# Kernel tuning notes

Measured on AMD Instinct MI355X. Metric: run time of the kernel, lower is better.

Reference implementation:

```python
import jax, jax.numpy as jnp
import numpy as np

EPS = 1e-6
H = 12  # heads

def layernorm(x, alpha, bias):
    # Faithful to source: unbiased std (ddof=1) and division by (std + eps)
    mean = jnp.mean(x, axis=-1, keepdims=True)
    std = jnp.std(x, axis=-1, ddof=1, keepdims=True)
    return alpha * (x - mean) / (std + EPS) + bias

def setup_inputs() -> dict:
    key = jax.random.key(0)
    ks = jax.random.split(key, 8)
    B, S, D, F = 2, 2048, 768, 3072
    w_scale = 0.02  # keep activations in a sane range
    return {
        "x": jax.random.normal(ks[0], (B, S, D), dtype=jnp.float32),
        "src_mask": jnp.ones((B, 1, 1, S), dtype=jnp.int32),
        "wq": jax.random.normal(ks[1], (D, D), dtype=jnp.float32) * w_scale,
        "wk": jax.random.normal(ks[2], (D, D), dtype=jnp.float32) * w_scale,
        "wv": jax.random.normal(ks[3], (D, D), dtype=jnp.float32) * w_scale,
        "wo": jax.random.normal(ks[4], (D, D), dtype=jnp.float32) * w_scale,
        "w1": jax.random.normal(ks[5], (D, F), dtype=jnp.float32) * w_scale,
        "b1": jnp.zeros((F,), dtype=jnp.float32),
        "w2": jax.random.normal(ks[6], (F, D), dtype=jnp.float32) * w_scale,
        "b2": jnp.zeros((D,), dtype=jnp.float32),
        "ln1_alpha": jnp.ones((1,), dtype=jnp.float32),
        "ln1_bias": jnp.zeros((1,), dtype=jnp.float32),
        "ln2_alpha": jnp.ones((1,), dtype=jnp.float32),
        "ln2_bias": jnp.zeros((1,), dtype=jnp.float32),
    }

def reference(x, src_mask, wq, wk, wv, wo, w1, b1, w2, b2,
              ln1_alpha, ln1_bias, ln2_alpha, ln2_bias):
    B, S, D = x.shape
    dk = D // H
    # ---- residual 1: pre-LN self-attention ----
    t = layernorm(x, ln1_alpha, ln1_bias)
    q = (t @ wq).reshape(B, S, H, dk).transpose(0, 2, 1, 3)  # [B,H,S,dk]
    k = (t @ wk).reshape(B, S, H, dk).transpose(0, 2, 1, 3)
    v = (t @ wv).reshape(B, S, H, dk).transpose(0, 2, 1, 3)
    scores = jnp.einsum('bhqd,bhkd->bhqk', q, k) / jnp.sqrt(jnp.float32(dk))
    # Faithful to source quirk: masked positions are SET to 1e-9 (not -inf)
    scores = jnp.where(src_mask == 0, jnp.float32(1e-9), scores)
    attn = jax.nn.softmax(scores, axis=-1)
    o = jnp.einsum('bhqk,bhkd->bhqd', attn, v)
    o = o.transpose(0, 2, 1, 3).reshape(B, S, D) @ wo
    x = x + o
    # ---- residual 2: pre-LN FFN ----
    t = layernorm(x, ln2_alpha, ln2_bias)
    ffn = jax.nn.relu(t @ w1 + b1) @ w2 + b2
    return x + ffn
```

## Files before the change

### kernel.cpp

```cpp
#include <hip/hip_runtime.h>

#define AS1 __attribute__((address_space(1)))
#define AS3 __attribute__((address_space(3)))

typedef float f32x4 __attribute__((ext_vector_type(4)));
typedef __bf16 bf16x8 __attribute__((ext_vector_type(8)));

__device__ __forceinline__ unsigned short f2bf(float f) {
    union { float f; unsigned u; } v; v.f = f;
    unsigned r = v.u + 0x7fffu + ((v.u >> 16) & 1u);
    return (unsigned short)(r >> 16);
}

__device__ __forceinline__ void async16(const void* g, void* l) {
    __builtin_amdgcn_global_load_lds((AS1 void*)g, (AS3 void*)l, 16, 0, 0);
}

#define SWZ4(r) ((((r) & 3) ^ (((r) >> 2) & 3)))

__global__ void transpose_cvt(const float* __restrict__ W, unsigned short* __restrict__ Wt,
                              int K, int N) {
    __shared__ float tile[32][33];
    int n0 = blockIdx.x * 32, k0 = blockIdx.y * 32;
    int tx = threadIdx.x, ty = threadIdx.y;
#pragma unroll
    for (int i = 0; i < 32; i += 8)
        tile[ty + i][tx] = W[(size_t)(k0 + ty + i) * N + n0 + tx];
    __syncthreads();
#pragma unroll
    for (int i = 0; i < 32; i += 8)
        Wt[(size_t)(n0 + ty + i) * K + k0 + tx] = f2bf(tile[tx][ty + i]);
}

__global__ __launch_bounds__(256) void ln_kernel(const float* __restrict__ x,
                                                 unsigned short* __restrict__ t,
                                                 const float* __restrict__ alpha,
                                                 const float* __restrict__ bias) {
    const int row = blockIdx.x;
    const float* xr = x + (size_t)row * 768;
    float v[3], sum = 0.f, ss = 0.f;
#pragma unroll
    for (int i = 0; i < 3; i++) {
        v[i] = xr[threadIdx.x + 256 * i];
        sum += v[i]; ss += v[i] * v[i];
    }
#pragma unroll
    for (int off = 32; off; off >>= 1) {
        sum += __shfl_down(sum, off);
        ss  += __shfl_down(ss, off);
    }
    __shared__ float s1[4], s2[4];
    int wid = threadIdx.x >> 6, lane = threadIdx.x & 63;
    if (lane == 0) { s1[wid] = sum; s2[wid] = ss; }
    __syncthreads();
    if (threadIdx.x == 0) {
        float a = 0.f, b = 0.f;
#pragma unroll
        for (int i = 0; i < 4; i++) { a += s1[i]; b += s2[i]; }
        s1[0] = a; s2[0] = b;
    }
    __syncthreads();
    sum = s1[0]; ss = s2[0];
    float mean = sum * (1.f / 768.f);
    float var = (ss - sum * mean) * (1.f / 767.f);
    float sc = alpha[0] / (sqrtf(fmaxf(var, 0.f)) + 1e-6f);
    float bs = bias[0];
#pragma unroll
    for (int i = 0; i < 3; i++)
        t[(size_t)row * 768 + threadIdx.x + 256 * i] = f2bf(sc * (v[i] - mean) + bs);
}

template <int MODE>
__global__ __launch_bounds__(256, 2) void gemm_bt(
    const unsigned short* __restrict__ A, const unsigned short* __restrict__ Bt,
    int M, int N, int K, const float* __restrict__ bias,
    const float* __restrict__ res, void* __restrict__ outp) {
    __shared__ __align__(16) unsigned short As[128 * 32];
    __shared__ __align__(16) unsigned short Bs[128 * 32];
    const int tid = threadIdx.x;
    const int lane = tid & 63, w = tid >> 6;
    const int wm = w & 1, wn = w >> 1;
    const int m0 = blockIdx.y * 128, n0 = blockIdx.x * 128;
    const int quad = lane >> 4, l16 = lane & 15;

    const int s0 = (2 * w) * 64 + lane;
    const int r0 = s0 >> 2, g0 = s0 & 3;
    const int s1 = s0 + 64;
    const int r1 = s1 >> 2, g1 = s1 & 3;
    const unsigned short* gA0 = A  + (size_t)(m0 + r0) * K + ((g0 ^ SWZ4(r0)) * 8);
    const unsigned short* gA1 = A  + (size_t)(m0 + r1) * K + ((g1 ^ SWZ4(r1)) * 8);
    const unsigned short* gB0 = Bt + (size_t)(n0 + r0) * K + ((g0 ^ SWZ4(r0)) * 8);
    const unsigned short* gB1 = Bt + (size_t)(n0 + r1) * K + ((g1 ^ SWZ4(r1)) * 8);
    unsigned short* lA0 = As + (2 * w) * 512;
    unsigned short* lA1 = As + (2 * w + 1) * 512;
    unsigned short* lB0 = Bs + (2 * w) * 512;
    unsigned short* lB1 = Bs + (2 * w + 1) * 512;

    f32x4 acc[4][4];
    const f32x4 z = {0.f, 0.f, 0.f, 0.f};
#pragma unroll
    for (int mt = 0; mt < 4; mt++)
#pragma unroll
        for (int nt = 0; nt < 4; nt++) acc[mt][nt] = z;

    const int nK = K >> 5;
    for (int kt = 0; kt < nK; ++kt) {
        __syncthreads();
        async16(gA0, lA0); async16(gA1, lA1);
        async16(gB0, lB0); async16(gB1, lB1);
        gA0 += 32; gA1 += 32; gB0 += 32; gB1 += 32;
        __syncthreads();
        bf16x8 af[4], bf[4];
#pragma unroll
        for (int mt = 0; mt < 4; mt++) {
            int r = 64 * wm + 16 * mt + l16;
            af[mt] = *(const bf16x8*)&As[r * 32 + ((quad ^ SWZ4(r)) * 8)];
        }
#pragma unroll
        for (int nt = 0; nt < 4; nt++) {
            int r = 64 * wn + 16 * nt + l16;
            bf[nt] = *(const bf16x8*)&Bs[r * 32 + ((quad ^ SWZ4(r)) * 8)];
        }
#pragma unroll
        for (int mt = 0; mt < 4; mt++)
#pragma unroll
            for (int nt = 0; nt < 4; nt++)
                acc[mt][nt] = __builtin_amdgcn_mfma_f32_16x16x32_bf16(af[mt], bf[nt], acc[mt][nt], 0, 0, 0);
    }

#pragma unroll
    for (int mt = 0; mt < 4; mt++) {
#pragma unroll
        for (int nt = 0; nt < 4; nt++) {
            const int col = n0 + 64 * wn + 16 * nt + l16;
            float bv = 0.f;
            if (MODE == 1 || MODE == 3) bv = bias[col];
#pragma unroll
            for (int r = 0; r < 4; r++) {
                const int row = m0 + 64 * wm + 16 * mt + quad * 4 + r;
                const size_t idx = (size_t)row * N + col;
                const float v = acc[mt][nt][r];
                if (MODE == 0) ((unsigned short*)outp)[idx] = f2bf(v);
                else if (MODE == 1) ((unsigned short*)outp)[idx] = f2bf(fmaxf(v + bv, 0.f));
                else if (MODE == 2) ((float*)outp)[idx] = v + res[idx];
                else ((float*)outp)[idx] = v + bv + res[idx];
            }
        }
    }
}

template <int MODE>
__global__ __launch_bounds__(256, 3) void gemm64_bt(
    const unsigned short* __restrict__ A, const unsigned short* __restrict__ Bt,
    int M, int N, int K, const float* __restrict__ bias,
    const float* __restrict__ res, void* __restrict__ outp) {
    __shared__ __align__(16) unsigned short As[64 * 32];
    __shared__ __align__(16) unsigned short Bs[64 * 32];
    const int tid = threadIdx.x;
    const int lane = tid & 63, w = tid >> 6;
    const int m0 = blockIdx.y * 64, n0 = blockIdx.x * 64;
    const int quad = lane >> 4, l16 = lane & 15;

    const int sl = w * 64 + lane;
    const int r = sl >> 2, g = sl & 3;
    const unsigned short* gA = A  + (size_t)(m0 + r) * K + ((g ^ SWZ4(r)) * 8);
    const unsigned short* gB = Bt + (size_t)(n0 + r) * K + ((g ^ SWZ4(r)) * 8);
    unsigned short* lA = As + w * 512;
    unsigned short* lB = Bs + w * 512;

    f32x4 acc[4];
    const f32x4 z = {0.f, 0.f, 0.f, 0.f};
#pragma unroll
    for (int nt = 0; nt < 4; nt++) acc[nt] = z;

    const int nK = K >> 5;
    for (int kt = 0; kt < nK; ++kt) {
        __syncthreads();
        async16(gA, lA); async16(gB, lB);
        gA += 32; gB += 32;
        __syncthreads();
        const int ra = 16 * w + l16;
        bf16x8 af = *(const bf16x8*)&As[ra * 32 + ((quad ^ SWZ4(ra)) * 8)];
#pragma unroll
        for (int nt = 0; nt < 4; nt++) {
            int rb = 16 * nt + l16;
            bf16x8 bf = *(const bf16x8*)&Bs[rb * 32 + ((quad ^ SWZ4(rb)) * 8)];
            acc[nt] = __builtin_amdgcn_mfma_f32_16x16x32_bf16(af, bf, acc[nt], 0, 0, 0);
        }
    }

#pragma unroll
    for (int nt = 0; nt < 4; nt++) {
        const int col = n0 + 16 * nt + l16;
        float bv = 0.f;
        if (MODE == 1 || MODE == 3) bv = bias[col];
#pragma unroll
        for (int rr = 0; rr < 4; rr++) {
            const int row = m0 + 16 * w + quad * 4 + rr;
            const size_t idx = (size_t)row * N + col;
            const float v = acc[nt][rr];
            if (MODE == 0) ((unsigned short*)outp)[idx] = f2bf(v);
            else if (MODE == 1) ((unsigned short*)outp)[idx] = f2bf(fmaxf(v + bv, 0.f));
            else if (MODE == 2) ((float*)outp)[idx] = v + res[idx];
            else ((float*)outp)[idx] = v + bv + res[idx];
        }
    }
}

__global__ void v_transpose(const unsigned short* __restrict__ qkvc,
                            unsigned short* __restrict__ vt) {
    __shared__ unsigned short t[64][65];
    const int bh = blockIdx.y, b = bh / 12, h = bh % 12;
    const int s0 = blockIdx.x * 64;
    const int tx = threadIdx.x, ty = threadIdx.y;
#pragma unroll
    for (int i = 0; i < 64; i += 4)
        t[ty + i][tx] = qkvc[(size_t)(b * 2048 + s0 + ty + i) * 2304 + 1536 + h * 64 + tx];
    __syncthreads();
#pragma unroll
    for (int i = 0; i < 64; i += 4)
        vt[((size_t)bh * 64 + ty + i) * 2048 + s0 + tx] = t[tx][ty + i];
}

__global__ __launch_bounds__(256, 3) void flash_attn(
    const unsigned short* __restrict__ qkvc,
    const unsigned short* __restrict__ vt,
    const int* __restrict__ mask,
    unsigned short* __restrict__ attno) {
    const int bh = blockIdx.y, b = bh / 12, h = bh % 12;
    const int s0 = blockIdx.x * 64;
    __shared__ __align__(16) unsigned short UQP[4 * 16 * 136];
    __shared__ __align__(16) unsigned short Ks[128 * 64];
    __shared__ __align__(16) unsigned short Vs[64 * 128];
    __shared__ int Ms[128];
    const int tid = threadIdx.x, lane = tid & 63, w = tid >> 6;
    const int quad = lane >> 4, l16 = lane & 15;

    {
        int sl0 = (2 * w) * 64 + lane;
        int r0 = sl0 >> 3, g0 = sl0 & 7;
        int sl1 = sl0 + 64;
        int r1 = sl1 >> 3, g1 = sl1 & 7;
        async16(qkvc + (size_t)(b * 2048 + s0 + r0) * 2304 + h * 64 + ((g0 ^ (r0 & 7)) * 8),
                UQP + (2 * w) * 512);
        async16(qkvc + (size_t)(b * 2048 + s0 + r1) * 2304 + h * 64 + ((g1 ^ (r1 & 7)) * 8),
                UQP + (2 * w + 1) * 512);
    }
    __syncthreads();
    bf16x8 aQ[2];
    {
        int r = 16 * w + l16;
#pragma unroll
        for (int kk = 0; kk < 2; kk++)
            aQ[kk] = *(const bf16x8*)&UQP[r * 64 + (((kk * 4 + quad) ^ (r & 7)) * 8)];
    }
    __bf16* Ps = (__bf16*)(UQP + w * (16 * 136));

    f32x4 Oacc[4], Lacc;
    const f32x4 z = {0.f, 0.f, 0.f, 0.f};
#pragma unroll
    for (int nt = 0; nt < 4; nt++) Oacc[nt] = z;
    Lacc = z;
    bf16x8 ones;
#pragma unroll
    for (int i = 0; i < 8; i++) ones[i] = (__bf16)1.0f;

    const unsigned short* kbase = qkvc + 768;
    const unsigned short* vbase = vt + (size_t)bh * 64 * 2048;
    const float SCL = 0.125f * 1.44269504088896340736f;
    const float MSK = 1.4426950408889634e-9f;

    for (int j = 0; j < 16; j++) {
        const int k0 = j * 128;
        __syncthreads();
#pragma unroll
        for (int c = 0; c < 4; c++) {
            int sl = (4 * w + c) * 64 + lane;
            int r = sl >> 3, g = sl & 7;
            async16(kbase + (size_t)(b * 2048 + k0 + r) * 2304 + h * 64 + ((g ^ (r & 7)) * 8),
                    Ks + (4 * w + c) * 512);
        }
#pragma unroll
        for (int c = 0; c < 4; c++) {
            int sl = (4 * w + c) * 64 + lane;
            int r = sl >> 4, g = sl & 15;
            async16(vbase + (size_t)r * 2048 + k0 + ((g ^ (r & 15)) * 8),
                    Vs + (4 * w + c) * 512);
        }
        if (tid < 128) Ms[tid] = mask[b * 2048 + k0 + tid];
        __syncthreads();

        f32x4 sc[8];
#pragma unroll
        for (int nt = 0; nt < 8; nt++) {
            int rr = nt * 16 + l16;
            bf16x8 bk0 = *(const bf16x8*)&Ks[rr * 64 + (((0 + quad) ^ (rr & 7)) * 8)];
            bf16x8 bk1 = *(const bf16x8*)&Ks[rr * 64 + (((4 + quad) ^ (rr & 7)) * 8)];
            sc[nt] = __builtin_amdgcn_mfma_f32_16x16x32_bf16(aQ[0], bk0, z, 0, 0, 0);
            sc[nt] = __builtin_amdgcn_mfma_f32_16x16x32_bf16(aQ[1], bk1, sc[nt], 0, 0, 0);
        }
#pragma unroll
        for (int nt = 0; nt < 8; nt++) {
            const int msk = Ms[nt * 16 + l16];
#pragma unroll
            for (int r = 0; r < 4; r++) {
                float v = msk ? sc[nt][r] * SCL : MSK;
                sc[nt][r] = __builtin_amdgcn_exp2f(v);
            }
        }
#pragma unroll
        for (int nt = 0; nt < 8; nt++)
#pragma unroll
            for (int r = 0; r < 4; r++)
                Ps[(quad * 4 + r) * 136 + nt * 16 + l16] = (__bf16)sc[nt][r];

#pragma unroll
        for (int ktile = 0; ktile < 4; ktile++) {
            bf16x8 aP = *(const bf16x8*)&Ps[l16 * 136 + ktile * 32 + quad * 8];
            Lacc = __builtin_amdgcn_mfma_f32_16x16x32_bf16(aP, ones, Lacc, 0, 0, 0);
#pragma unroll
            for (int nt = 0; nt < 4; nt++) {
                int rr = nt * 16 + l16;
                bf16x8 bv = *(const bf16x8*)&Vs[rr * 128 + (((ktile * 4 + quad) ^ (rr & 15)) * 8)];
                Oacc[nt] = __builtin_amdgcn_mfma_f32_16x16x32_bf16(aP, bv, Oacc[nt], 0, 0, 0);
            }
        }
    }

    float inv[4];
#pragma unroll
    for (int r = 0; r < 4; r++) inv[r] = 1.0f / Lacc[r];
#pragma unroll
    for (int nt = 0; nt < 4; nt++)
#pragma unroll
        for (int r = 0; r < 4; r++) {
            const int row = s0 + 16 * w + quad * 4 + r;
            attno[(size_t)(b * 2048 + row) * 768 + h * 64 + nt * 16 + l16] =
                f2bf(Oacc[nt][r] * inv[r]);
        }
}

extern "C" void kernel_launch(void* const* d_in, const int* in_sizes, int n_in,
                              void* d_out, int out_size, void* d_ws, size_t ws_size,
                              hipStream_t stream) {
    const float* x    = (const float*)d_in[0];
    const int*   mask = (const int*)d_in[1];
    const float* wq   = (const float*)d_in[2];
    const float* wk   = (const float*)d_in[3];
    const float* wv   = (const float*)d_in[4];
    const float* wo   = (const float*)d_in[5];
    const float* w1   = (const float*)d_in[6];
    const float* b1   = (const float*)d_in[7];
    const float* w2   = (const float*)d_in[8];
    const float* b2   = (const float*)d_in[9];
    const float* ln1a = (const float*)d_in[10];
    const float* ln1b = (const float*)d_in[11];
    const float* ln2a = (const float*)d_in[12];
    const float* ln2b = (const float*)d_in[13];

    char* p = (char*)d_ws;
    auto carve = [&](size_t bytes) {
        char* q = p;
        p += (bytes + 255) & ~(size_t)255;
        return q;
    };
    unsigned short* wTqkv = (unsigned short*)carve((size_t)2304 * 768 * 2);
    unsigned short* wTo   = (unsigned short*)carve((size_t)768 * 768 * 2);
    unsigned short* wT1   = (unsigned short*)carve((size_t)3072 * 768 * 2);
    unsigned short* wT2   = (unsigned short*)carve((size_t)768 * 3072 * 2);
    unsigned short* vtb   = (unsigned short*)carve((size_t)24 * 64 * 2048 * 2);
    float*          x1    = (float*)carve((size_t)4096 * 768 * 4);
    char* unionA = carve((size_t)4096 * 768 * 2 + (size_t)4096 * 2304 * 2);
    unsigned short* t1   = (unsigned short*)unionA;
    unsigned short* qkvc = (unsigned short*)(unionA + (size_t)4096 * 768 * 2);
    unsigned short* ffnh = (unsigned short*)unionA;
    unsigned short* attno = (unsigned short*)carve((size_t)4096 * 768 * 2);
    unsigned short* t2 = attno;

    dim3 tb(32, 8);
    transpose_cvt<<<dim3(24, 24), tb, 0, stream>>>(wq, wTqkv, 768, 768);
    transpose_cvt<<<dim3(24, 24), tb, 0, stream>>>(wk, wTqkv + (size_t)768 * 768, 768, 768);
    transpose_cvt<<<dim3(24, 24), tb, 0, stream>>>(wv, wTqkv + (size_t)1536 * 768, 768, 768);
    transpose_cvt<<<dim3(24, 24), tb, 0, stream>>>(wo, wTo, 768, 768);
    transpose_cvt<<<dim3(96, 24), tb, 0, stream>>>(w1, wT1, 768, 3072);
    transpose_cvt<<<dim3(24, 96), tb, 0, stream>>>(w2, wT2, 3072, 768);

    ln_kernel<<<4096, 256, 0, stream>>>(x, t1, ln1a, ln1b);
    gemm_bt<0><<<dim3(18, 32), 256, 0, stream>>>(t1, wTqkv, 4096, 2304, 768,
                                                 nullptr, nullptr, qkvc);
    v_transpose<<<dim3(32, 24), dim3(64, 4), 0, stream>>>(qkvc, vtb);
    flash_attn<<<dim3(32, 24), 256, 0, stream>>>(qkvc, vtb, mask, attno);
    gemm64_bt<2><<<dim3(12, 64), 256, 0, stream>>>(attno, wTo, 4096, 768, 768,
                                                   nullptr, x, x1);
    ln_kernel<<<4096, 256, 0, stream>>>(x1, t2, ln2a, ln2b);
    gemm_bt<1><<<dim3(24, 32), 256, 0, stream>>>(t2, wT1, 4096, 3072, 768,
                                                 b1, nullptr, ffnh);
    gemm64_bt<3><<<dim3(12, 64), 256, 0, stream>>>(ffnh, wT2, 4096, 768, 3072,
                                                   b2, x1, (float*)d_out);
}
```

Before: 306.9 us.

## Double-buffer GEMM LDS tiles with register prefetch, one barrier per k-step

Both GEMM kernels switch from direct global-to-LDS async loads with two barriers per k-step to register-staged prefetch into double-buffered LDS with a single waitcnt+barrier. The next tile's global loads are issued before the current tile's MFMAs, aiming to hide global latency and halve barrier count. The 64x64 kernel also widens its K step from 32 to 64 using an 8-way XOR swizzle, and the 128 kernel's occupancy hint rises from 2 to 3 blocks. The trade-off is more registers for staging, double the LDS footprint, and a possible spill or occupancy loss under the tighter launch bound.

```diff
diff --git a/kernel.cpp b/kernel.cpp
--- a/kernel.cpp
+++ b/kernel.cpp
@@ -1,7 +1,4 @@
 #include <hip/hip_runtime.h>
-
-#define AS1 __attribute__((address_space(1)))
-#define AS3 __attribute__((address_space(3)))
 
 typedef float f32x4 __attribute__((ext_vector_type(4)));
 typedef __bf16 bf16x8 __attribute__((ext_vector_type(8)));
@@ -12,8 +9,14 @@
     return (unsigned short)(r >> 16);
 }
 
+#define AS1 __attribute__((address_space(1)))
+#define AS3 __attribute__((address_space(3)))
 __device__ __forceinline__ void async16(const void* g, void* l) {
     __builtin_amdgcn_global_load_lds((AS1 void*)g, (AS3 void*)l, 16, 0, 0);
+}
+
+__device__ __forceinline__ void sync_lds() {
+    asm volatile("s_waitcnt lgkmcnt(0)\n\ts_barrier" ::: "memory");
 }
 
 #define SWZ4(r) ((((r) & 3) ^ (((r) >> 2) & 3)))
@@ -71,30 +74,26 @@
 }
 
 template <int MODE>
-__global__ __launch_bounds__(256, 2) void gemm_bt(
+__global__ __launch_bounds__(256, 3) void gemm_bt(
     const unsigned short* __restrict__ A, const unsigned short* __restrict__ Bt,
     int M, int N, int K, const float* __restrict__ bias,
     const float* __restrict__ res, void* __restrict__ outp) {
-    __shared__ __align__(16) unsigned short As[128 * 32];
-    __shared__ __align__(16) unsigned short Bs[128 * 32];
+    __shared__ __align__(16) unsigned short As[2][128 * 32];
+    __shared__ __align__(16) unsigned short Bs[2][128 * 32];
     const int tid = threadIdx.x;
     const int lane = tid & 63, w = tid >> 6;
     const int wm = w & 1, wn = w >> 1;
     const int m0 = blockIdx.y * 128, n0 = blockIdx.x * 128;
     const int quad = lane >> 4, l16 = lane & 15;
 
-    const int s0 = (2 * w) * 64 + lane;
-    const int r0 = s0 >> 2, g0 = s0 & 3;
-    const int s1 = s0 + 64;
-    const int r1 = s1 >> 2, g1 = s1 & 3;
-    const unsigned short* gA0 = A  + (size_t)(m0 + r0) * K + ((g0 ^ SWZ4(r0)) * 8);
-    const unsigned short* gA1 = A  + (size_t)(m0 + r1) * K + ((g1 ^ SWZ4(r1)) * 8);
-    const unsigned short* gB0 = Bt + (size_t)(n0 + r0) * K + ((g0 ^ SWZ4(r0)) * 8);
-    const unsigned short* gB1 = Bt + (size_t)(n0 + r1) * K + ((g1 ^ SWZ4(r1)) * 8);
-    unsigned short* lA0 = As + (2 * w) * 512;
-    unsigned short* lA1 = As + (2 * w + 1) * 512;
-    unsigned short* lB0 = Bs + (2 * w) * 512;
-    unsigned short* lB1 = Bs + (2 * w + 1) * 512;
+    const int r0 = tid >> 2, g0 = tid & 3;
+    const int r1 = r0 + 64, g1 = g0;
+    const unsigned short* gA0 = A  + (size_t)(m0 + r0) * K + g0 * 8;
+    const unsigned short* gA1 = A  + (size_t)(m0 + r1) * K + g1 * 8;
+    const unsigned short* gB0 = Bt + (size_t)(n0 + r0) * K + g0 * 8;
+    const unsigned short* gB1 = Bt + (size_t)(n0 + r1) * K + g1 * 8;
+    const int wA0 = r0 * 32 + ((g0 ^ SWZ4(r0)) * 8);
+    const int wA1 = r1 * 32 + ((g1 ^ SWZ4(r1)) * 8);
 
     f32x4 acc[4][4];
     const f32x4 z = {0.f, 0.f, 0.f, 0.f};
@@ -103,23 +102,32 @@
 #pragma unroll
         for (int nt = 0; nt < 4; nt++) acc[mt][nt] = z;
 
+    bf16x8 ra0 = *(const bf16x8*)gA0, ra1 = *(const bf16x8*)gA1;
+    bf16x8 rb0 = *(const bf16x8*)gB0, rb1 = *(const bf16x8*)gB1;
+    gA0 += 32; gA1 += 32; gB0 += 32; gB1 += 32;
+
     const int nK = K >> 5;
     for (int kt = 0; kt < nK; ++kt) {
-        __syncthreads();
-        async16(gA0, lA0); async16(gA1, lA1);
-        async16(gB0, lB0); async16(gB1, lB1);
-        gA0 += 32; gA1 += 32; gB0 += 32; gB1 += 32;
-        __syncthreads();
+        unsigned short* Ac = As[kt & 1];
+        unsigned short* Bc = Bs[kt & 1];
+        *(bf16x8*)&Ac[wA0] = ra0; *(bf16x8*)&Ac[wA1] = ra1;
+        *(bf16x8*)&Bc[wA0] = rb0; *(bf16x8*)&Bc[wA1] = rb1;
+        if (kt + 1 < nK) {
+            ra0 = *(const bf16x8*)gA0; ra1 = *(const bf16x8*)gA1;
+            rb0 = *(const bf16x8*)gB0; rb1 = *(const bf16x8*)gB1;
+            gA0 += 32; gA1 += 32; gB0 += 32; gB1 += 32;
+        }
+        sync_lds();
         bf16x8 af[4], bf[4];
 #pragma unroll
         for (int mt = 0; mt < 4; mt++) {
             int r = 64 * wm + 16 * mt + l16;
-            af[mt] = *(const bf16x8*)&As[r * 32 + ((quad ^ SWZ4(r)) * 8)];
+            af[mt] = *(const bf16x8*)&Ac[r * 32 + ((quad ^ SWZ4(r)) * 8)];
         }
 #pragma unroll
         for (int nt = 0; nt < 4; nt++) {
             int r = 64 * wn + 16 * nt + l16;
-            bf[nt] = *(const bf16x8*)&Bs[r * 32 + ((quad ^ SWZ4(r)) * 8)];
+            bf[nt] = *(const bf16x8*)&Bc[r * 32 + ((quad ^ SWZ4(r)) * 8)];
         }
 #pragma unroll
         for (int mt = 0; mt < 4; mt++)
@@ -154,38 +162,53 @@
     const unsigned short* __restrict__ A, const unsigned short* __restrict__ Bt,
     int M, int N, int K, const float* __restrict__ bias,
     const float* __restrict__ res, void* __restrict__ outp) {
-    __shared__ __align__(16) unsigned short As[64 * 32];
-    __shared__ __align__(16) unsigned short Bs[64 * 32];
+    __shared__ __align__(16) unsigned short As[2][64 * 64];
+    __shared__ __align__(16) unsigned short Bs[2][64 * 64];
     const int tid = threadIdx.x;
     const int lane = tid & 63, w = tid >> 6;
     const int m0 = blockIdx.y * 64, n0 = blockIdx.x * 64;
     const int quad = lane >> 4, l16 = lane & 15;
 
-    const int sl = w * 64 + lane;
-    const int r = sl >> 2, g = sl & 3;
-    const unsigned short* gA = A  + (size_t)(m0 + r) * K + ((g ^ SWZ4(r)) * 8);
-    const unsigned short* gB = Bt + (size_t)(n0 + r) * K + ((g ^ SWZ4(r)) * 8);
-    unsigned short* lA = As + w * 512;
-    unsigned short* lB = Bs + w * 512;
+    const int r0 = tid >> 3, g0 = tid & 7;
+    const int r1 = r0 + 32, g1 = g0;
+    const unsigned short* gA0 = A  + (size_t)(m0 + r0) * K + g0 * 8;
+    const unsigned short* gA1 = A  + (size_t)(m0 + r1) * K + g1 * 8;
+    const unsigned short* gB0 = Bt + (size_t)(n0 + r0) * K + g0 * 8;
+    const unsigned short* gB1 = Bt + (size_t)(n0 + r1) * K + g1 * 8;
+    const int wA0 = r0 * 64 + ((g0 ^ (r0 & 7)) * 8);
+    const int wA1 = r1 * 64 + ((g1 ^ (r1 & 7)) * 8);
 
     f32x4 acc[4];
     const f32x4 z = {0.f, 0.f, 0.f, 0.f};
 #pragma unroll
     for (int nt = 0; nt < 4; nt++) acc[nt] = z;
 
-    const int nK = K >> 5;
+    bf16x8 ra0 = *(const bf16x8*)gA0, ra1 = *(const bf16x8*)gA1;
+    bf16x8 rb0 = *(const bf16x8*)gB0, rb1 = *(const bf16x8*)gB1;
+    gA0 += 64; gA1 += 64; gB0 += 64; gB1 += 64;
+
+    const int nK = K >> 6;
     for (int kt = 0; kt < nK; ++kt) {
-        __syncthreads();
-        async16(gA, lA); async16(gB, lB);
-        gA += 32; gB += 32;
-        __syncthreads();
+        unsigned short* Ac = As[kt & 1];
+        unsigned short* Bc = Bs[kt & 1];
+        *(bf16x8*)&Ac[wA0] = ra0; *(bf16x8*)&Ac[wA1] = ra1;
+        *(bf16x8*)&Bc[wA0] = rb0; *(bf16x8*)&Bc[wA1] = rb1;
+        if (kt + 1 < nK) {
+            ra0 = *(const bf16x8*)gA0; ra1 = *(const bf16x8*)gA1;
+            rb0 = *(const bf16x8*)gB0; rb1 = *(const bf16x8*)gB1;
+            gA0 += 64; gA1 += 64; gB0 += 64; gB1 += 64;
+        }
+        sync_lds();
         const int ra = 16 * w + l16;
-        bf16x8 af = *(const bf16x8*)&As[ra * 32 + ((quad ^ SWZ4(ra)) * 8)];
+        bf16x8 af0 = *(const bf16x8*)&Ac[ra * 64 + (((0 + quad) ^ (ra & 7)) * 8)];
+        bf16x8 af1 = *(const bf16x8*)&Ac[ra * 64 + (((4 + quad) ^ (ra & 7)) * 8)];
 #pragma unroll
         for (int nt = 0; nt < 4; nt++) {
             int rb = 16 * nt + l16;
-            bf16x8 bf = *(const bf16x8*)&Bs[rb * 32 + ((quad ^ SWZ4(rb)) * 8)];
-            acc[nt] = __builtin_amdgcn_mfma_f32_16x16x32_bf16(af, bf, acc[nt], 0, 0, 0);
+            bf16x8 bf0 = *(const bf16x8*)&Bc[rb * 64 + (((0 + quad) ^ (rb & 7)) * 8)];
+            bf16x8 bf1 = *(const bf16x8*)&Bc[rb * 64 + (((4 + quad) ^ (rb & 7)) * 8)];
+            acc[nt] = __builtin_amdgcn_mfma_f32_16x16x32_bf16(af0, bf0, acc[nt], 0, 0, 0);
+            acc[nt] = __builtin_amdgcn_mfma_f32_16x16x32_bf16(af1, bf1, acc[nt], 0, 0, 0);
         }
     }
 
```

Result: faster. 280.1 us (-8.7%).
